# Kernel tuning notes

Hardware: AMD Instinct MI355X
Metric: run time of the kernel (lower is better)

## Reference

```python
import jax, jax.numpy as jnp
import numpy as np

D_MODEL = 1024
H = 16
D = D_MODEL // H  # 64 per head
D_FF = 4096
LN_EPS = 1e-5


def layer_norm(x, gamma, beta):
    mu = jnp.mean(x, axis=-1, keepdims=True)
    var = jnp.mean(jnp.square(x - mu), axis=-1, keepdims=True)
    return (x - mu) * jax.lax.rsqrt(var + LN_EPS) * gamma + beta


def setup_inputs() -> dict:
    key = jax.random.key(0)
    ks = jax.random.split(key, 12)
    s = 1.0 / np.sqrt(D_MODEL)
    sf = 1.0 / np.sqrt(D_FF)
    return {
        "x": jax.random.normal(ks[0], (2, 2048, D_MODEL), jnp.float32),
        "src_mask": 0,
        "w_q": jax.random.normal(ks[1], (D_MODEL, D_MODEL), jnp.float32) * s,
        "w_k": jax.random.normal(ks[2], (D_MODEL, D_MODEL), jnp.float32) * s,
        "w_v": jax.random.normal(ks[3], (D_MODEL, D_MODEL), jnp.float32) * s,
        "w_0": jax.random.normal(ks[4], (D_MODEL, D_MODEL), jnp.float32) * s,
        "b_0": jnp.zeros((D_MODEL,), jnp.float32),
        "w_1": jax.random.normal(ks[5], (D_MODEL, D_FF), jnp.float32) * s,
        "b_1": jnp.zeros((D_FF,), jnp.float32),
        "w_2": jax.random.normal(ks[6], (D_FF, D_MODEL), jnp.float32) * sf,
        "b_2": jnp.zeros((D_MODEL,), jnp.float32),
        "g_1": jnp.ones((D_MODEL,), jnp.float32),
        "be_1": jnp.zeros((D_MODEL,), jnp.float32),
        "g_2": jnp.ones((D_MODEL,), jnp.float32),
        "be_2": jnp.zeros((D_MODEL,), jnp.float32),
    }


def reference(x, src_mask, w_q, w_k, w_v, w_0, b_0, w_1, b_1, w_2, b_2, g_1, be_1, g_2, be_2):
    N, S, _ = x.shape
    # --- pre-LN self-attention branch ---
    x_n = layer_norm(x, g_1, be_1)
    q = (x_n @ w_q).reshape(N, S, H, D).transpose(0, 2, 1, 3)  # [N,H,S,D]
    k = (x_n @ w_k).reshape(N, S, H, D).transpose(0, 2, 1, 3)
    v = (x_n @ w_v).reshape(N, S, H, D).transpose(0, 2, 1, 3)
    scores = jnp.einsum('nhqd,nhkd->nhqk', q, k) / np.sqrt(D)
    # src_mask == 0 (falsy) in the original -> no masking applied
    attn = jax.nn.softmax(scores, axis=-1)
    out = jnp.einsum('nhqk,nhkd->nhqd', attn, v)
    out = out.transpose(0, 2, 1, 3).reshape(N, S, H * D)
    attn_out = out @ w_0 + b_0
    x = x + attn_out  # dropout is identity in eval
    # --- pre-LN feedforward branch ---
    x_n = layer_norm(x, g_2, be_2)
    ff = jax.nn.relu(x_n @ w_1 + b_1) @ w_2 + b_2
    return x + ff
```

## Files before the change

### kernel.cpp

```cpp
#include <hip/hip_runtime.h>

typedef __bf16 bf16x8 __attribute__((ext_vector_type(8)));
typedef float f32x4 __attribute__((ext_vector_type(4)));
typedef unsigned short u16x8 __attribute__((ext_vector_type(8)));
typedef unsigned short u16x4 __attribute__((ext_vector_type(4)));

__device__ __forceinline__ unsigned short f2bf_bits(float f) {
  unsigned u = __float_as_uint(f);
  return (unsigned short)((u + 0x7FFFu + ((u >> 16) & 1u)) >> 16);
}

__device__ __forceinline__ float exp2_amd(float x) {
  return __builtin_amdgcn_exp2f(x);
}

__device__ __forceinline__ unsigned cvt_pk_bf16(float a, float b) {
  unsigned r;
  asm("v_cvt_pk_bf16_f32 %0, %1, %2" : "=v"(r) : "v"(a), "v"(b));
  return r;
}

__device__ __forceinline__ float red16_max(float x) {
  unsigned a = __float_as_uint(x), b = a;
  asm("v_permlane16_swap_b32 %0, %1" : "+v"(a), "+v"(b));
  return fmaxf(__uint_as_float(a), __uint_as_float(b));
}
__device__ __forceinline__ float red32_max(float x) {
  unsigned a = __float_as_uint(x), b = a;
  asm("v_permlane32_swap_b32 %0, %1" : "+v"(a), "+v"(b));
  return fmaxf(__uint_as_float(a), __uint_as_float(b));
}
__device__ __forceinline__ float red16_sum(float x) {
  unsigned a = __float_as_uint(x), b = a;
  asm("v_permlane16_swap_b32 %0, %1" : "+v"(a), "+v"(b));
  return __uint_as_float(a) + __uint_as_float(b);
}
__device__ __forceinline__ float red32_sum(float x) {
  unsigned a = __float_as_uint(x), b = a;
  asm("v_permlane32_swap_b32 %0, %1" : "+v"(a), "+v"(b));
  return __uint_as_float(a) + __uint_as_float(b);
}

__device__ __forceinline__ void gload16(const void* g, void* l) {
  __builtin_amdgcn_global_load_lds(
      (const __attribute__((address_space(1))) unsigned int*)g,
      (__attribute__((address_space(3))) unsigned int*)l, 16, 0, 0);
}

__global__ __launch_bounds__(256) void wconv_t(const float* __restrict__ src,
                                               unsigned short* __restrict__ dst,
                                               int R, int C) {
  __shared__ float tile[32][33];
  const int tx = threadIdx.x & 31, ty = threadIdx.x >> 5;
  const size_t c0 = (size_t)blockIdx.x * 32, r0 = (size_t)blockIdx.y * 32;
#pragma unroll
  for (int i = 0; i < 4; i++)
    tile[ty + i * 8][tx] = src[(r0 + ty + i * 8) * C + c0 + tx];
  __syncthreads();
#pragma unroll
  for (int i = 0; i < 4; i++) {
    int c = ty + i * 8;
    dst[(c0 + c) * R + r0 + tx] = f2bf_bits(tile[tx][c]);
  }
}

__global__ __launch_bounds__(256) void ln_k(const float* __restrict__ x,
                                            const float* __restrict__ g,
                                            const float* __restrict__ be,
                                            unsigned short* __restrict__ o) {
  const int row = blockIdx.x, tid = threadIdx.x;
  const float4 v = ((const float4*)(x + (size_t)row * 1024))[tid];
  float s = v.x + v.y + v.z + v.w;
  float s2 = v.x * v.x + v.y * v.y + v.z * v.z + v.w * v.w;
#pragma unroll
  for (int m = 1; m < 64; m <<= 1) {
    s += __shfl_xor(s, m);
    s2 += __shfl_xor(s2, m);
  }
  __shared__ float red[8];
  const int w = tid >> 6;
  if ((tid & 63) == 0) { red[w] = s; red[4 + w] = s2; }
  __syncthreads();
  s = red[0] + red[1] + red[2] + red[3];
  s2 = red[4] + red[5] + red[6] + red[7];
  const float mu = s * (1.f / 1024.f);
  const float rs_ = rsqrtf(s2 * (1.f / 1024.f) - mu * mu + 1e-5f);
  const float4 gg = ((const float4*)g)[tid];
  const float4 bb = ((const float4*)be)[tid];
  u16x4 pack;
  pack.x = f2bf_bits((v.x - mu) * rs_ * gg.x + bb.x);
  pack.y = f2bf_bits((v.y - mu) * rs_ * gg.y + bb.y);
  pack.z = f2bf_bits((v.z - mu) * rs_ * gg.z + bb.z);
  pack.w = f2bf_bits((v.w - mu) * rs_ * gg.w + bb.w);
  *(u16x4*)(o + (size_t)row * 1024 + tid * 4) = pack;
}

__global__ __launch_bounds__(256) void ff2red(const float* __restrict__ p,
                                              const float* __restrict__ bias,
                                              const float* __restrict__ res,
                                              float* __restrict__ out) {
  const size_t i = ((size_t)blockIdx.x * 256 + threadIdx.x) * 8;
  const int col = (int)(i & 1023);
  const float4 b0 = *(const float4*)(bias + col);
  const float4 b1 = *(const float4*)(bias + col + 4);
  const float4 r0 = *(const float4*)(res + i);
  const float4 r1 = *(const float4*)(res + i + 4);
  const float4 p00 = *(const float4*)(p + i);
  const float4 p01 = *(const float4*)(p + i + 4);
  const float4 p10 = *(const float4*)(p + 4194304 + i);
  const float4 p11 = *(const float4*)(p + 4194304 + i + 4);
  float4 o0 = {b0.x + r0.x + p00.x + p10.x, b0.y + r0.y + p00.y + p10.y,
               b0.z + r0.z + p00.z + p10.z, b0.w + r0.w + p00.w + p10.w};
  float4 o1 = {b1.x + r1.x + p01.x + p11.x, b1.y + r1.y + p01.y + p11.y,
               b1.z + r1.z + p01.z + p11.z, b1.w + r1.w + p01.w + p11.w};
  *(float4*)(out + i) = o0;
  *(float4*)(out + i + 4) = o1;
}

template <int EPI>
__global__ __launch_bounds__(256) void gemm_bt(
    const unsigned short* __restrict__ A, const unsigned short* __restrict__ Bt,
    const float* __restrict__ bias, const float* __restrict__ res,
    void* __restrict__ Cv, int M, int N, int K, int KL) {
  __shared__ __align__(16) unsigned short As[2][128 * 64];
  __shared__ __align__(16) unsigned short Bs[2][128 * 64];
  const int tid = threadIdx.x, lane = tid & 63, w = tid >> 6;
  const int lo = lane & 15, hi = lane >> 4;
  const int l8 = lane >> 3, l7 = lane & 7;
  const int scol = ((l7 ^ l8) << 3);
  const int nwg = gridDim.x * gridDim.y;
  int bid = blockIdx.y * gridDim.x + blockIdx.x;
  if ((nwg & 7) == 0) bid = (bid & 7) * (nwg >> 3) + (bid >> 3);
  const int bx = bid % gridDim.x, by = bid / gridDim.x;
  const size_t rowBase = (size_t)by * 128;
  const size_t colBase = (size_t)bx * 128;
  const int kOff = blockIdx.z * KL;
  f32x4 acc[4][4];
#pragma unroll
  for (int i = 0; i < 4; i++)
#pragma unroll
    for (int j = 0; j < 4; j++) acc[i][j] = (f32x4){0.f, 0.f, 0.f, 0.f};
  const int wr = (w >> 1) * 64, wc = (w & 1) * 64;
  const unsigned short* aSrc = A + (rowBase + (size_t)w * 32 + l8) * K + scol + kOff;
  const unsigned short* bSrc = Bt + (colBase + (size_t)w * 32 + l8) * K + scol + kOff;

  const int NT = KL >> 6;
  auto stage = [&](int t, int buf) {
    const int kb = t << 6;
#pragma unroll
    for (int c = 0; c < 4; c++) {
      gload16(aSrc + (size_t)c * 8 * K + kb, &As[buf][(w * 4 + c) * 512]);
      gload16(bSrc + (size_t)c * 8 * K + kb, &Bs[buf][(w * 4 + c) * 512]);
    }
  };

  stage(0, 0);
  stage(1, 1);
  asm volatile("s_waitcnt vmcnt(8)" ::: "memory");
  __builtin_amdgcn_s_barrier();

  for (int t = 0; t < NT; ++t) {
    const int cur = t & 1;
    const char* asb = (const char*)As[cur];
    const char* bsb = (const char*)Bs[cur];
    __builtin_amdgcn_s_setprio(1);
#pragma unroll
    for (int ks = 0; ks < 2; ks++) {
      bf16x8 af[4], bfr[4];
      const int kbyte = ks * 64 + (hi << 4);
#pragma unroll
      for (int i = 0; i < 4; i++) {
        const int ar = wr + i * 16 + lo;
        af[i] = *(const bf16x8*)(asb + ar * 128 + (kbyte ^ ((ar & 7) << 4)));
        const int br = wc + i * 16 + lo;
        bfr[i] = *(const bf16x8*)(bsb + br * 128 + (kbyte ^ ((br & 7) << 4)));
      }
#pragma unroll
      for (int i = 0; i < 4; i++)
#pragma unroll
        for (int j = 0; j < 4; j++)
          acc[i][j] = __builtin_amdgcn_mfma_f32_16x16x32_bf16(af[i], bfr[j], acc[i][j], 0, 0, 0);
    }
    __builtin_amdgcn_s_setprio(0);
    asm volatile("s_waitcnt lgkmcnt(0)" ::: "memory");
    __builtin_amdgcn_s_barrier();
    if (t + 2 < NT) {
      stage(t + 2, cur);
      asm volatile("s_waitcnt vmcnt(8)" ::: "memory");
    } else {
      asm volatile("s_waitcnt vmcnt(0)" ::: "memory");
    }
    __builtin_amdgcn_s_barrier();
  }

  const size_t zOff = (size_t)blockIdx.z * M * N;
#pragma unroll
  for (int i = 0; i < 4; i++) {
#pragma unroll
    for (int r = 0; r < 4; r++) {
      const size_t row = rowBase + wr + i * 16 + hi * 4 + r;
#pragma unroll
      for (int j = 0; j < 4; j++) {
        const size_t col = colBase + wc + j * 16 + lo;
        float v = acc[i][j][r];
        if (EPI == 1) {
          ((float*)Cv)[row * N + col] = v + bias[col] + res[row * N + col];
        } else if (EPI == 2) {
          ((unsigned short*)Cv)[row * N + col] = f2bf_bits(fmaxf(v + bias[col], 0.f));
        } else if (EPI == 3) {
          ((float*)Cv)[zOff + row * N + col] = v;
        } else {
          ((unsigned short*)Cv)[row * N + col] = f2bf_bits(v);
        }
      }
    }
  }
}

__global__ __launch_bounds__(256) void attn_k(const unsigned short* __restrict__ Q,
                                              const unsigned short* __restrict__ K,
                                              const unsigned short* __restrict__ V,
                                              unsigned short* __restrict__ O) {
  __shared__ __align__(16) unsigned short Ks[2][64 * 64];
  __shared__ __align__(16) unsigned short Vt[2][64 * 64];
  const int tid = threadIdx.x, lane = tid & 63, w = tid >> 6;
  const int lo = lane & 15, hi = lane >> 4;
  const int l8 = lane >> 3, l7 = lane & 7;
  const int scol = ((l7 ^ l8) << 3);
  const int b = blockIdx.x;
  const int qt = b >> 5;
  const int hn = (b & 7) + 8 * ((b >> 3) & 3);
  const int h = hn & 15, n = hn >> 4;
  const size_t tRow0 = (size_t)n * 2048;
  const int colBase = h * 64;
  const int LD = 3072;
  const float SC = 0.125f * 1.44269504f;

  const unsigned short* qrowA = Q + (tRow0 + qt * 128 + w * 32 + lo) * LD + colBase;
  const unsigned short* qrowB = qrowA + 16 * LD;
  const bf16x8 qf[2][2] = {
      {*(const bf16x8*)(qrowA + hi * 8), *(const bf16x8*)(qrowA + 32 + hi * 8)},
      {*(const bf16x8*)(qrowB + hi * 8), *(const bf16x8*)(qrowB + 32 + hi * 8)}};
  float m2[2] = {-1e30f, -1e30f}, l_r[2] = {0.f, 0.f};
  f32x4 oacc[2][4];
#pragma unroll
  for (int g = 0; g < 2; g++)
#pragma unroll
    for (int d = 0; d < 4; d++) oacc[g][d] = (f32x4){0.f, 0.f, 0.f, 0.f};

  const int vkv = tid & 63, vdg = tid >> 6;
  const unsigned short* vbase = V + (tRow0 + vkv) * LD + colBase + vdg * 16;
  const unsigned short* kbase = K + (tRow0 + (size_t)w * 16 + l8) * LD + colBase + scol;

  u16x8 v0 = *(const u16x8*)(vbase);
  u16x8 v1 = *(const u16x8*)(vbase + 8);
#pragma unroll
  for (int c = 0; c < 2; c++)
    gload16(kbase + (size_t)c * 8 * LD, &Ks[0][(w * 2 + c) * 512]);
  {
    char* vt = (char*)Vt[0];
#pragma unroll
    for (int j = 0; j < 8; j++) {
      *(unsigned short*)(vt + (vdg * 16 + j) * 128 + ((vkv * 2) ^ (j << 4))) = v0[j];
      *(unsigned short*)(vt + (vdg * 16 + 8 + j) * 128 + ((vkv * 2) ^ (j << 4))) = v1[j];
    }
  }
  __syncthreads();

  for (int t = 0; t < 32; ++t) {
    const int cur = t & 1;
    if (t < 31) {
      v0 = *(const u16x8*)(vbase + (size_t)(t + 1) * 64 * LD);
      v1 = *(const u16x8*)(vbase + (size_t)(t + 1) * 64 * LD + 8);
#pragma unroll
      for (int c = 0; c < 2; c++)
        gload16(kbase + ((size_t)(t + 1) * 64 + c * 8) * LD, &Ks[cur ^ 1][(w * 2 + c) * 512]);
    }
    f32x4 s[2][4];
    const char* ksb = (const char*)Ks[cur];
    __builtin_amdgcn_s_setprio(1);
#pragma unroll
    for (int f = 0; f < 4; f++) {
      const int kr = f * 16 + lo;
      const bf16x8 b0 = *(const bf16x8*)(ksb + kr * 128 + ((hi * 16) ^ ((kr & 7) << 4)));
      const bf16x8 b1 = *(const bf16x8*)(ksb + kr * 128 + ((64 + hi * 16) ^ ((kr & 7) << 4)));
#pragma unroll
      for (int g = 0; g < 2; g++) {
        s[g][f] = __builtin_amdgcn_mfma_f32_16x16x32_bf16(b0, qf[g][0], (f32x4){0.f, 0.f, 0.f, 0.f}, 0, 0, 0);
        s[g][f] = __builtin_amdgcn_mfma_f32_16x16x32_bf16(b1, qf[g][1], s[g][f], 0, 0, 0);
      }
    }
    __builtin_amdgcn_s_setprio(0);
    unsigned W2[2][4][2];
#pragma unroll
    for (int g = 0; g < 2; g++) {
      float mx = fmaxf(fmaxf(fmaxf(s[g][0][0], s[g][0][1]), fmaxf(s[g][0][2], s[g][0][3])),
                       fmaxf(fmaxf(s[g][1][0], s[g][1][1]), fmaxf(s[g][1][2], s[g][1][3])));
      mx = fmaxf(mx, fmaxf(fmaxf(fmaxf(s[g][2][0], s[g][2][1]), fmaxf(s[g][2][2], s[g][2][3])),
                           fmaxf(fmaxf(s[g][3][0], s[g][3][1]), fmaxf(s[g][3][2], s[g][3][3]))));
      mx = red16_max(mx);
      mx = red32_max(mx);
      const float mx2v = mx * SC;
      if (__any(mx2v > m2[g] + 8.f)) {
        const float mn = fmaxf(m2[g], mx2v);
        const float al = exp2_amd(m2[g] - mn);
        l_r[g] *= al;
        m2[g] = mn;
#pragma unroll
        for (int r = 0; r < 4; r++) {
          const float alr = __shfl(al, hi * 4 + r);
#pragma unroll
          for (int d = 0; d < 4; d++) oacc[g][d][r] *= alr;
        }
      }
      float p[4][4];
      float lsum = 0.f;
#pragma unroll
      for (int f = 0; f < 4; f++)
#pragma unroll
        for (int r = 0; r < 4; r++) {
          p[f][r] = exp2_amd(fmaf(s[g][f][r], SC, -m2[g]));
          lsum += p[f][r];
        }
      l_r[g] += lsum;
#pragma unroll
      for (int f = 0; f < 4; f++) {
        W2[g][f][0] = cvt_pk_bf16(p[f][0], p[f][1]);
        W2[g][f][1] = cvt_pk_bf16(p[f][2], p[f][3]);
      }
    }
    __builtin_amdgcn_s_setprio(1);
#pragma unroll
    for (int ks = 0; ks < 2; ks++) {
      union { unsigned u[4]; bf16x8 v; } apu[2];
#pragma unroll
      for (int g = 0; g < 2; g++) {
        unsigned wa[2], wb[2];
#pragma unroll
        for (int hh = 0; hh < 2; hh++) {
          unsigned X = W2[g][ks * 2][hh], Y = W2[g][ks * 2 + 1][hh];
          asm("v_permlane32_swap_b32 %0, %1" : "+v"(X), "+v"(Y));
          const unsigned Bx = __shfl_xor((int)Y, 16);
          const unsigned Ax = __shfl_xor((int)X, 16);
          wa[hh] = (hi & 1) ? Bx : X;
          wb[hh] = (hi & 1) ? Y : Ax;
        }
        apu[g].u[0] = wa[0]; apu[g].u[1] = wa[1]; apu[g].u[2] = wb[0]; apu[g].u[3] = wb[1];
      }
      const int kbyte = ks * 64 + (hi << 4);
#pragma unroll
      for (int d = 0; d < 4; d++) {
        const int dr = d * 16 + lo;
        const bf16x8 bv = *(const bf16x8*)((const char*)Vt[cur] + dr * 128 + (kbyte ^ ((dr & 7) << 4)));
        oacc[0][d] = __builtin_amdgcn_mfma_f32_16x16x32_bf16(apu[0].v, bv, oacc[0][d], 0, 0, 0);
        oacc[1][d] = __builtin_amdgcn_mfma_f32_16x16x32_bf16(apu[1].v, bv, oacc[1][d], 0, 0, 0);
      }
    }
    __builtin_amdgcn_s_setprio(0);
    if (t < 31) {
      char* vt = (char*)Vt[cur ^ 1];
#pragma unroll
      for (int j = 0; j < 8; j++) {
        *(unsigned short*)(vt + (vdg * 16 + j) * 128 + ((vkv * 2) ^ (j << 4))) = v0[j];
        *(unsigned short*)(vt + (vdg * 16 + 8 + j) * 128 + ((vkv * 2) ^ (j << 4))) = v1[j];
      }
    }
    __syncthreads();
  }
#pragma unroll
  for (int g = 0; g < 2; g++) {
    const float l = red32_sum(red16_sum(l_r[g]));
    const float inv = 1.f / l;
#pragma unroll
    for (int r = 0; r < 4; r++) {
      const float invr = __shfl(inv, hi * 4 + r);
      const size_t row = tRow0 + qt * 128 + w * 32 + g * 16 + hi * 4 + r;
#pragma unroll
      for (int d = 0; d < 4; d++)
        O[row * 1024 + colBase + d * 16 + lo] = f2bf_bits(oacc[g][d][r] * invr);
    }
  }
}

extern "C" void kernel_launch(void* const* d_in, const int* in_sizes, int n_in,
                              void* d_out, int out_size, void* d_ws, size_t ws_size,
                              hipStream_t stream) {
  (void)in_sizes; (void)n_in; (void)out_size; (void)ws_size;
  const float* x   = (const float*)d_in[0];
  const float* w_q = (const float*)d_in[2];
  const float* w_k = (const float*)d_in[3];
  const float* w_v = (const float*)d_in[4];
  const float* w_0 = (const float*)d_in[5];
  const float* b_0 = (const float*)d_in[6];
  const float* w_1 = (const float*)d_in[7];
  const float* b_1 = (const float*)d_in[8];
  const float* w_2 = (const float*)d_in[9];
  const float* b_2 = (const float*)d_in[10];
  const float* g_1 = (const float*)d_in[11];
  const float* be_1 = (const float*)d_in[12];
  const float* g_2 = (const float*)d_in[13];
  const float* be_2 = (const float*)d_in[14];

  char* ws = (char*)d_ws;
  size_t off = 0;
  auto alloc = [&](size_t bytes) {
    void* p = ws + off;
    off += (bytes + 255) & ~(size_t)255;
    return p;
  };
  const size_t MB = 1024 * 1024;
  unsigned short* wt_q = (unsigned short*)alloc(2 * MB);
  unsigned short* wt_k = (unsigned short*)alloc(2 * MB);
  unsigned short* wt_v = (unsigned short*)alloc(2 * MB);
  unsigned short* wt_0 = (unsigned short*)alloc(2 * MB);
  unsigned short* wt_1 = (unsigned short*)alloc(8 * MB);
  unsigned short* wt_2 = (unsigned short*)alloc(8 * MB);
  unsigned short* xn   = (unsigned short*)alloc(8 * MB);
  unsigned short* qkv  = (unsigned short*)alloc(24 * MB);
  unsigned short* aO   = (unsigned short*)alloc(8 * MB);
  float*          x1f  = (float*)alloc(16 * MB);
  unsigned short* ff1  = (unsigned short*)alloc(32 * MB);
  float* part = (float*)qkv;

  wconv_t<<<dim3(32, 32), 256, 0, stream>>>(w_q, wt_q, 1024, 1024);
  wconv_t<<<dim3(32, 32), 256, 0, stream>>>(w_k, wt_k, 1024, 1024);
  wconv_t<<<dim3(32, 32), 256, 0, stream>>>(w_v, wt_v, 1024, 1024);
  wconv_t<<<dim3(32, 32), 256, 0, stream>>>(w_0, wt_0, 1024, 1024);
  wconv_t<<<dim3(128, 32), 256, 0, stream>>>(w_1, wt_1, 1024, 4096);
  wconv_t<<<dim3(32, 128), 256, 0, stream>>>(w_2, wt_2, 4096, 1024);

  ln_k<<<4096, 256, 0, stream>>>(x, g_1, be_1, xn);
  gemm_bt<0><<<dim3(24, 32), 256, 0, stream>>>(xn, wt_q, nullptr, nullptr, qkv, 4096, 3072, 1024, 1024);
  attn_k<<<512, 256, 0, stream>>>(qkv, qkv + 1024, qkv + 2048, aO);
  gemm_bt<1><<<dim3(8, 32), 256, 0, stream>>>(aO, wt_0, b_0, x, x1f, 4096, 1024, 1024, 1024);
  ln_k<<<4096, 256, 0, stream>>>(x1f, g_2, be_2, xn);
  gemm_bt<2><<<dim3(32, 32), 256, 0, stream>>>(xn, wt_1, b_1, nullptr, ff1, 4096, 4096, 1024, 1024);
  gemm_bt<3><<<dim3(8, 32, 2), 256, 0, stream>>>(ff1, wt_2, nullptr, nullptr, part, 4096, 1024, 4096, 2048);
  ff2red<<<2048, 256, 0, stream>>>(part, b_2, x1f, (float*)d_out);
}
```

Baseline: 259.6 us.

## Split-K the output projection, fuse reduction with LayerNorm, merge weight conversions

The six weight-transpose launches become one kernel that picks its source matrix from the block index. The W0 projection GEMM now runs split-K with two partial buffers, doubling its block count from 256 to 512. A new kernel sums the partials, adds bias and residual, and applies the second LayerNorm in the same pass, which removes the separate ln_k launch and a re-read of x1f. The cost is an extra write and read of the fp32 partial buffers, which reuse the ff1 workspace.

```diff
diff --git a/kernel.cpp b/kernel.cpp
--- a/kernel.cpp
+++ b/kernel.cpp
@@ -47,12 +47,32 @@
       (__attribute__((address_space(3))) unsigned int*)l, 16, 0, 0);
 }
 
-__global__ __launch_bounds__(256) void wconv_t(const float* __restrict__ src,
-                                               unsigned short* __restrict__ dst,
-                                               int R, int C) {
+__global__ __launch_bounds__(256) void wconv_all(
+    const float* __restrict__ s0, const float* __restrict__ s1,
+    const float* __restrict__ s2, const float* __restrict__ s3,
+    const float* __restrict__ s4, const float* __restrict__ s5,
+    unsigned short* __restrict__ d0, unsigned short* __restrict__ d1,
+    unsigned short* __restrict__ d2, unsigned short* __restrict__ d3,
+    unsigned short* __restrict__ d4, unsigned short* __restrict__ d5) {
+  const int t = blockIdx.x;
+  const float* src;
+  unsigned short* dst;
+  int R, C, bx, by;
+  if (t < 4096) {
+    const int i = t >> 10, id = t & 1023;
+    src = i == 0 ? s0 : i == 1 ? s1 : i == 2 ? s2 : s3;
+    dst = i == 0 ? d0 : i == 1 ? d1 : i == 2 ? d2 : d3;
+    R = 1024; C = 1024; bx = id & 31; by = id >> 5;
+  } else if (t < 8192) {
+    const int id = t - 4096;
+    src = s4; dst = d4; R = 1024; C = 4096; bx = id & 127; by = id >> 7;
+  } else {
+    const int id = t - 8192;
+    src = s5; dst = d5; R = 4096; C = 1024; bx = id & 31; by = id >> 5;
+  }
   __shared__ float tile[32][33];
   const int tx = threadIdx.x & 31, ty = threadIdx.x >> 5;
-  const size_t c0 = (size_t)blockIdx.x * 32, r0 = (size_t)blockIdx.y * 32;
+  const size_t c0 = (size_t)bx * 32, r0 = (size_t)by * 32;
 #pragma unroll
   for (int i = 0; i < 4; i++)
     tile[ty + i * 8][tx] = src[(r0 + ty + i * 8) * C + c0 + tx];
@@ -93,6 +113,50 @@
   pack.z = f2bf_bits((v.z - mu) * rs_ * gg.z + bb.z);
   pack.w = f2bf_bits((v.w - mu) * rs_ * gg.w + bb.w);
   *(u16x4*)(o + (size_t)row * 1024 + tid * 4) = pack;
+}
+
+__global__ __launch_bounds__(256) void w0red_ln(const float* __restrict__ p,
+                                                const float* __restrict__ b0,
+                                                const float* __restrict__ x,
+                                                const float* __restrict__ g,
+                                                const float* __restrict__ be,
+                                                float* __restrict__ x1f,
+                                                unsigned short* __restrict__ xn) {
+  const int row = blockIdx.x, tid = threadIdx.x;
+  const size_t base = (size_t)row * 1024 + tid * 4;
+  const float4 xv = *(const float4*)(x + base);
+  const float4 bb0 = ((const float4*)b0)[tid];
+  const float4 p0 = *(const float4*)(p + base);
+  const float4 p1 = *(const float4*)(p + 4194304 + base);
+  float4 v;
+  v.x = xv.x + bb0.x + p0.x + p1.x;
+  v.y = xv.y + bb0.y + p0.y + p1.y;
+  v.z = xv.z + bb0.z + p0.z + p1.z;
+  v.w = xv.w + bb0.w + p0.w + p1.w;
+  *(float4*)(x1f + base) = v;
+  float s = v.x + v.y + v.z + v.w;
+  float s2 = v.x * v.x + v.y * v.y + v.z * v.z + v.w * v.w;
+#pragma unroll
+  for (int m = 1; m < 64; m <<= 1) {
+    s += __shfl_xor(s, m);
+    s2 += __shfl_xor(s2, m);
+  }
+  __shared__ float red[8];
+  const int w = tid >> 6;
+  if ((tid & 63) == 0) { red[w] = s; red[4 + w] = s2; }
+  __syncthreads();
+  s = red[0] + red[1] + red[2] + red[3];
+  s2 = red[4] + red[5] + red[6] + red[7];
+  const float mu = s * (1.f / 1024.f);
+  const float rs_ = rsqrtf(s2 * (1.f / 1024.f) - mu * mu + 1e-5f);
+  const float4 gg = ((const float4*)g)[tid];
+  const float4 bb = ((const float4*)be)[tid];
+  u16x4 pack;
+  pack.x = f2bf_bits((v.x - mu) * rs_ * gg.x + bb.x);
+  pack.y = f2bf_bits((v.y - mu) * rs_ * gg.y + bb.y);
+  pack.z = f2bf_bits((v.z - mu) * rs_ * gg.z + bb.z);
+  pack.w = f2bf_bits((v.w - mu) * rs_ * gg.w + bb.w);
+  *(u16x4*)(xn + base) = pack;
 }
 
 __global__ __launch_bounds__(256) void ff2red(const float* __restrict__ p,
@@ -203,9 +267,7 @@
       for (int j = 0; j < 4; j++) {
         const size_t col = colBase + wc + j * 16 + lo;
         float v = acc[i][j][r];
-        if (EPI == 1) {
-          ((float*)Cv)[row * N + col] = v + bias[col] + res[row * N + col];
-        } else if (EPI == 2) {
+        if (EPI == 2) {
           ((unsigned short*)Cv)[row * N + col] = f2bf_bits(fmaxf(v + bias[col], 0.f));
         } else if (EPI == 3) {
           ((float*)Cv)[zOff + row * N + col] = v;
@@ -420,21 +482,17 @@
   unsigned short* aO   = (unsigned short*)alloc(8 * MB);
   float*          x1f  = (float*)alloc(16 * MB);
   unsigned short* ff1  = (unsigned short*)alloc(32 * MB);
-  float* part = (float*)qkv;
-
-  wconv_t<<<dim3(32, 32), 256, 0, stream>>>(w_q, wt_q, 1024, 1024);
-  wconv_t<<<dim3(32, 32), 256, 0, stream>>>(w_k, wt_k, 1024, 1024);
-  wconv_t<<<dim3(32, 32), 256, 0, stream>>>(w_v, wt_v, 1024, 1024);
-  wconv_t<<<dim3(32, 32), 256, 0, stream>>>(w_0, wt_0, 1024, 1024);
-  wconv_t<<<dim3(128, 32), 256, 0, stream>>>(w_1, wt_1, 1024, 4096);
-  wconv_t<<<dim3(32, 128), 256, 0, stream>>>(w_2, wt_2, 4096, 1024);
-
+  float* w0part  = (float*)ff1;
+  float* ff2part = (float*)qkv;
+
+  wconv_all<<<12288, 256, 0, stream>>>(w_q, w_k, w_v, w_0, w_1, w_2,
+                                       wt_q, wt_k, wt_v, wt_0, wt_1, wt_2);
   ln_k<<<4096, 256, 0, stream>>>(x, g_1, be_1, xn);
   gemm_bt<0><<<dim3(24, 32), 256, 0, stream>>>(xn, wt_q, nullptr, nullptr, qkv, 4096, 3072, 1024, 1024);
   attn_k<<<512, 256, 0, stream>>>(qkv, qkv + 1024, qkv + 2048, aO);
-  gemm_bt<1><<<dim3(8, 32), 256, 0, stream>>>(aO, wt_0, b_0, x, x1f, 4096, 1024, 1024, 1024);
-  ln_k<<<4096, 256, 0, stream>>>(x1f, g_2, be_2, xn);
+  gemm_bt<3><<<dim3(8, 32, 2), 256, 0, stream>>>(aO, wt_0, nullptr, nullptr, w0part, 4096, 1024, 1024, 512);
+  w0red_ln<<<4096, 256, 0, stream>>>(w0part, b_0, x, g_2, be_2, x1f, xn);
   gemm_bt<2><<<dim3(32, 32), 256, 0, stream>>>(xn, wt_1, b_1, nullptr, ff1, 4096, 4096, 1024, 1024);
-  gemm_bt<3><<<dim3(8, 32, 2), 256, 0, stream>>>(ff1, wt_2, nullptr, nullptr, part, 4096, 1024, 4096, 2048);
-  ff2red<<<2048, 256, 0, stream>>>(part, b_2, x1f, (float*)d_out);
-}
+  gemm_bt<3><<<dim3(8, 32, 2), 256, 0, stream>>>(ff1, wt_2, nullptr, nullptr, ff2part, 4096, 1024, 4096, 2048);
+  ff2red<<<2048, 256, 0, stream>>>(ff2part, b_2, x1f, (float*)d_out);
+}
```

Result: faster. 249.9 us (-3.8%).
